# Kernel tuning notes

Measured on AMD Instinct MI355X. Metric: run time of the kernel, lower is better.

## Reference

```python
import jax, jax.numpy as jnp
import numpy as np

E = 2048        # embed_dim
HQ = 32         # num_query_heads
HKV = 8         # num_kv_heads
HD = E // HQ    # head_dim = 64
GROUP = HQ // HKV  # q_per_kv = 4
B, T = 2, 2048


def setup_inputs() -> dict:
    key = jax.random.key(0)
    ks = jax.random.split(key, 6)
    s = 0.02
    x  = jax.random.normal(ks[0], (B, T, E), dtype=jnp.float32)
    Wq = jax.random.normal(ks[1], (E, E), dtype=jnp.float32) * s
    Wk = jax.random.normal(ks[2], (E, HKV * HD), dtype=jnp.float32) * s
    Wv = jax.random.normal(ks[3], (E, HKV * HD), dtype=jnp.float32) * s
    Wo = jax.random.normal(ks[4], (E, E), dtype=jnp.float32) * s
    bo = jax.random.normal(ks[5], (E,), dtype=jnp.float32) * s
    return {"x": x, "Wq": Wq, "Wk": Wk, "Wv": Wv, "Wo": Wo, "bo": bo}


def reference(x, Wq, Wk, Wv, Wo, bo):
    Bc, Tc, _ = x.shape
    # projections
    q = (x @ Wq).reshape(Bc, Tc, HQ, HD).transpose(0, 2, 1, 3)      # [B,HQ,T,HD]
    k = (x @ Wk).reshape(Bc, Tc, HKV, HD).transpose(0, 2, 1, 3)     # [B,HKV,T,HD]
    v = (x @ Wv).reshape(Bc, Tc, HKV, HD).transpose(0, 2, 1, 3)     # [B,HKV,T,HD]
    # group queries by kv head instead of repeating k/v: [B,HKV,GROUP,T,HD]
    qg = q.reshape(Bc, HKV, GROUP, Tc, HD)
    scale = 1.0 / jnp.sqrt(jnp.asarray(HD, dtype=x.dtype))
    scores = jnp.einsum('bhgqd,bhkd->bhgqk', qg, k) * scale         # [B,HKV,GROUP,T,T]
    weights = jax.nn.softmax(scores, axis=-1)
    attn = jnp.einsum('bhgqk,bhkd->bhgqd', weights, v)              # [B,HKV,GROUP,T,HD]
    out = attn.reshape(Bc, HQ, Tc, HD).transpose(0, 2, 1, 3).reshape(Bc, Tc, E)
    return out @ Wo + bo
```

## Files before the change

kernel.cpp:

```cpp
#include <hip/hip_runtime.h>
#include <hip/hip_bf16.h>
#include <stdint.h>

#define E_ 2048
#define HQ_ 32
#define HKV_ 8
#define HD_ 64
#define B_ 2
#define T_ 2048
#define MROWS (B_*T_)
#define NKV (HKV_*HD_)
#define NQKV (E_ + 2*NKV)
#define SCALE_LOG2E 0.18033688011112042f

typedef __bf16 bf16_t;
typedef __bf16 bf16x8 __attribute__((ext_vector_type(8)));
typedef float f32x4 __attribute__((ext_vector_type(4)));
typedef float f32x16 __attribute__((ext_vector_type(16)));

typedef const __attribute__((address_space(1))) unsigned int glb_u32;
typedef __attribute__((address_space(3))) unsigned int lds_u32;

__device__ __forceinline__ unsigned short f2bf_bits(float f) {
  unsigned int u = __float_as_uint(f);
  u += 0x7FFFu + ((u >> 16) & 1u);
  return (unsigned short)(u >> 16);
}
__device__ __forceinline__ bf16_t f2bf(float f) {
  union { unsigned short s; bf16_t h; } u;
  u.s = f2bf_bits(f);
  return u.h;
}
__device__ __forceinline__ unsigned pack2bf(float lo, float hi) {
  union { struct { bf16_t l, h; } s; unsigned u; } c;
  c.s.l = (bf16_t)lo; c.s.h = (bf16_t)hi;
  return c.u;
}
__device__ __forceinline__ float fexp2(float x) {
#if __has_builtin(__builtin_amdgcn_exp2f)
  return __builtin_amdgcn_exp2f(x);
#else
  return exp2f(x);
#endif
}

__global__ void cast_x_kernel(const float* __restrict__ in, bf16_t* __restrict__ out, int n8) {
  int i = blockIdx.x * blockDim.x + threadIdx.x;
  int stride = gridDim.x * blockDim.x;
  for (; i < n8; i += stride) {
    const float4* p = reinterpret_cast<const float4*>(in) + (size_t)i * 2;
    float4 a = p[0], b = p[1];
    union { unsigned short s[8]; uint4 v; } u;
    u.s[0] = f2bf_bits(a.x); u.s[1] = f2bf_bits(a.y);
    u.s[2] = f2bf_bits(a.z); u.s[3] = f2bf_bits(a.w);
    u.s[4] = f2bf_bits(b.x); u.s[5] = f2bf_bits(b.y);
    u.s[6] = f2bf_bits(b.z); u.s[7] = f2bf_bits(b.w);
    reinterpret_cast<uint4*>(out)[i] = u.v;
  }
}

__global__ void transpose_cast_w(const float* __restrict__ in, bf16_t* __restrict__ out,
                                 int R, int C) {
  __shared__ float tile[32][33];
  int c0 = blockIdx.x * 32, r0 = blockIdx.y * 32;
  int tx = threadIdx.x, ty = threadIdx.y;
#pragma unroll
  for (int j = 0; j < 4; ++j) {
    int r = ty + j * 8;
    tile[r][tx] = in[(size_t)(r0 + r) * C + c0 + tx];
  }
  __syncthreads();
#pragma unroll
  for (int j = 0; j < 4; ++j) {
    int c = ty + j * 8;
    out[(size_t)(c0 + c) * R + r0 + tx] = f2bf(tile[tx][c]);
  }
}

__global__ void transpose_v_kernel(const bf16_t* __restrict__ qkv, bf16_t* __restrict__ vt) {
  __shared__ bf16_t tile[32][33];
  int b = blockIdx.z;
  int hd0 = blockIdx.x * 32, t0 = blockIdx.y * 32;
  int tx = threadIdx.x, ty = threadIdx.y;
#pragma unroll
  for (int j = 0; j < 4; ++j) {
    int tt = ty + j * 8;
    tile[tt][tx] = qkv[(size_t)(b * T_ + t0 + tt) * NQKV + (E_ + NKV) + hd0 + tx];
  }
  __syncthreads();
#pragma unroll
  for (int j = 0; j < 4; ++j) {
    int hh = ty + j * 8;
    vt[(size_t)(b * NKV + hd0 + hh) * T_ + t0 + tx] = tile[tx][hh];
  }
}

template <int OUTMODE>
__global__ void gemm_bt_kernel(const bf16_t* __restrict__ A, const bf16_t* __restrict__ BT,
                               void* __restrict__ Cv, const float* __restrict__ bias,
                               int M, int N, int K) {
  __shared__ bf16_t As[128 * 32];
  __shared__ bf16_t Bs[128 * 32];
  int tid = threadIdx.x;
  int w = tid >> 6, lane = tid & 63;
  int l15 = lane & 15, l4 = lane >> 4;
  int m0 = blockIdx.x * 128, n0 = blockIdx.y * 128;
  int wm = (w >> 1) * 64, wn = (w & 1) * 64;

  f32x4 zero = {0.f, 0.f, 0.f, 0.f};
  f32x4 acc[4][4];
#pragma unroll
  for (int mt = 0; mt < 4; ++mt)
#pragma unroll
    for (int nt = 0; nt < 4; ++nt) acc[mt][nt] = zero;

  int nK = K >> 5;
  for (int kt = 0; kt < nK; ++kt) {
    int k0 = kt << 5;
#pragma unroll
    for (int j = 0; j < 2; ++j) {
      int c = w * 2 + j;
      int L = c * 512 + lane * 8;
      int row = L >> 5, col = L & 31;
      __builtin_amdgcn_global_load_lds((glb_u32*)(A + (size_t)(m0 + row) * K + k0 + col),
                                       (lds_u32*)(As + c * 512), 16, 0, 0);
      __builtin_amdgcn_global_load_lds((glb_u32*)(BT + (size_t)(n0 + row) * K + k0 + col),
                                       (lds_u32*)(Bs + c * 512), 16, 0, 0);
    }
    __syncthreads();

    bf16x8 afr[4], bfr[4];
#pragma unroll
    for (int t = 0; t < 4; ++t) {
      afr[t] = *reinterpret_cast<const bf16x8*>(As + (wm + t * 16 + l15) * 32 + l4 * 8);
      bfr[t] = *reinterpret_cast<const bf16x8*>(Bs + (wn + t * 16 + l15) * 32 + l4 * 8);
    }
#pragma unroll
    for (int mt = 0; mt < 4; ++mt)
#pragma unroll
      for (int nt = 0; nt < 4; ++nt)
        acc[mt][nt] = __builtin_amdgcn_mfma_f32_16x16x32_bf16(afr[mt], bfr[nt], acc[mt][nt], 0, 0, 0);
    __syncthreads();
  }

  if (OUTMODE == 0) {
    bf16_t* C = reinterpret_cast<bf16_t*>(Cv);
#pragma unroll
    for (int mt = 0; mt < 4; ++mt)
#pragma unroll
      for (int nt = 0; nt < 4; ++nt) {
        int n = n0 + wn + nt * 16 + l15;
#pragma unroll
        for (int r = 0; r < 4; ++r) {
          int m = m0 + wm + mt * 16 + l4 * 4 + r;
          C[(size_t)m * N + n] = f2bf(acc[mt][nt][r]);
        }
      }
  } else {
    float* C = reinterpret_cast<float*>(Cv);
#pragma unroll
    for (int mt = 0; mt < 4; ++mt)
#pragma unroll
      for (int nt = 0; nt < 4; ++nt) {
        int n = n0 + wn + nt * 16 + l15;
        float bb = bias[n];
#pragma unroll
        for (int r = 0; r < 4; ++r) {
          int m = m0 + wm + mt * 16 + l4 * 4 + r;
          C[(size_t)m * N + n] = acc[mt][nt][r] + bb;
        }
      }
  }
}

__global__ void attn_kernel(const bf16_t* __restrict__ qkv, const bf16_t* __restrict__ vt,
                            bf16_t* __restrict__ attn) {
  __shared__ bf16_t Kbuf[2][64 * 64];
  __shared__ bf16_t Vbuf[2][64 * 64];
  __shared__ float bcast[8][32];

  int tid = threadIdx.x;
  int w = tid >> 6, lane = tid & 63;
  int l31 = lane & 31, hi = lane >> 5;
  int bh = blockIdx.y;
  int b = bh >> 5, hq = bh & 31, hkv = hq >> 2;
  int q0 = blockIdx.x * 256 + w * 32;

  bf16x8 qf[4];
  {
    const bf16_t* qp = qkv + (size_t)(b * T_ + q0 + l31) * NQKV + hq * HD_;
#pragma unroll
    for (int s = 0; s < 4; ++s) {
      bf16x8 q = *reinterpret_cast<const bf16x8*>(qp + s * 16 + hi * 8);
#pragma unroll
      for (int e = 0; e < 8; ++e) q[e] = (bf16_t)((float)q[e] * SCALE_LOG2E);
      qf[s] = q;
    }
  }

  f32x16 o0 = {0.f,0.f,0.f,0.f,0.f,0.f,0.f,0.f,0.f,0.f,0.f,0.f,0.f,0.f,0.f,0.f};
  f32x16 o1 = o0;
  float m_r = -1e30f, l_r = 0.f;

  int srow = w * 8 + (lane >> 3);
  int schunk = (lane & 7) ^ ((lane >> 3) & 7);
  const bf16_t* kg = qkv + (size_t)b * T_ * NQKV + E_ + hkv * HD_;
  const bf16_t* vg = vt + ((size_t)(b * HKV_ + hkv) * HD_ + srow) * T_;

#define STAGE_KV(bi, kv0) do {                                                          \
    __builtin_amdgcn_global_load_lds(                                                   \
        (glb_u32*)(kg + (size_t)((kv0) + srow) * NQKV + schunk * 8),                    \
        (lds_u32*)(&Kbuf[bi][w * 8 * 64]), 16, 0, 0);                                   \
    __builtin_amdgcn_global_load_lds(                                                   \
        (glb_u32*)(vg + (kv0) + schunk * 8),                                            \
        (lds_u32*)(&Vbuf[bi][w * 8 * 64]), 16, 0, 0);                                   \
  } while (0)

#define KREAD(bi, tsub, s) \
  (*reinterpret_cast<const bf16x8*>(&Kbuf[bi][((tsub) * 32 + l31) * 64 + \
      ((((s) * 2 + hi) ^ (l31 & 7)) * 8)]))
#define VREAD(bi, dh, s) \
  (*reinterpret_cast<const bf16x8*>(&Vbuf[bi][((dh) * 32 + l31) * 64 + \
      ((((s) * 2 + hi) ^ (l31 & 7)) * 8)]))

  STAGE_KV(0, 0);
  __syncthreads();

#pragma unroll 2
  for (int t = 0; t < T_ / 64; ++t) {
    int bi = t & 1;
    if (t < T_ / 64 - 1) STAGE_KV(bi ^ 1, (t + 1) * 64);

    f32x16 sa = {0.f,0.f,0.f,0.f,0.f,0.f,0.f,0.f,0.f,0.f,0.f,0.f,0.f,0.f,0.f,0.f};
    f32x16 sb = sa;
    __builtin_amdgcn_s_setprio(1);
#pragma unroll
    for (int s = 0; s < 4; ++s) {
      sa = __builtin_amdgcn_mfma_f32_32x32x16_bf16(KREAD(bi, 0, s), qf[s], sa, 0, 0, 0);
      sb = __builtin_amdgcn_mfma_f32_32x32x16_bf16(KREAD(bi, 1, s), qf[s], sb, 0, 0, 0);
    }
    __builtin_amdgcn_s_setprio(0);

    float pmax = sa[0];
#pragma unroll
    for (int r = 1; r < 16; ++r) pmax = fmaxf(pmax, sa[r]);
#pragma unroll
    for (int r = 0; r < 16; ++r) pmax = fmaxf(pmax, sb[r]);

    if (__any(pmax > m_r + 8.f)) {
      float pm2 = __shfl_xor(pmax, 32);
      float mnew = fmaxf(m_r, fmaxf(pmax, pm2));
      float corr = fexp2(m_r - mnew);
      m_r = mnew;
      l_r *= corr;
      bcast[w][l31] = corr;
      asm volatile("s_waitcnt lgkmcnt(0)" ::: "memory");
#pragma unroll
      for (int r = 0; r < 16; ++r) {
        float c = bcast[w][(r & 3) + 8 * (r >> 2) + 4 * hi];
        o0[r] *= c; o1[r] *= c;
      }
    }

    float pA[16], pB[16];
    float ps0 = 0.f, ps1 = 0.f;
#pragma unroll
    for (int r = 0; r < 16; ++r) {
      pA[r] = fexp2(sa[r] - m_r); ps0 += pA[r];
      pB[r] = fexp2(sb[r] - m_r); ps1 += pB[r];
    }
    l_r += ps0 + ps1;

    unsigned wd[2][4][2];
#pragma unroll
    for (int g = 0; g < 4; ++g)
#pragma unroll
      for (int j = 0; j < 2; ++j) {
        wd[0][g][j] = pack2bf(pA[4 * g + 2 * j], pA[4 * g + 2 * j + 1]);
        wd[1][g][j] = pack2bf(pB[4 * g + 2 * j], pB[4 * g + 2 * j + 1]);
      }

    __builtin_amdgcn_s_setprio(1);
#pragma unroll
    for (int s = 0; s < 4; ++s) {
      const int tt = s >> 1, gg = 2 * (s & 1);
      unsigned send0 = hi ? wd[tt][gg][0] : wd[tt][gg + 1][0];
      unsigned send1 = hi ? wd[tt][gg][1] : wd[tt][gg + 1][1];
      unsigned recv0 = __shfl_xor(send0, 32);
      unsigned recv1 = __shfl_xor(send1, 32);
      union { unsigned u[4]; bf16x8 v; } pf;
      pf.u[0] = hi ? recv0 : wd[tt][gg][0];
      pf.u[1] = hi ? recv1 : wd[tt][gg][1];
      pf.u[2] = hi ? wd[tt][gg + 1][0] : recv0;
      pf.u[3] = hi ? wd[tt][gg + 1][1] : recv1;
      o0 = __builtin_amdgcn_mfma_f32_32x32x16_bf16(pf.v, VREAD(bi, 0, s), o0, 0, 0, 0);
      o1 = __builtin_amdgcn_mfma_f32_32x32x16_bf16(pf.v, VREAD(bi, 1, s), o1, 0, 0, 0);
    }
    __builtin_amdgcn_s_setprio(0);

    __syncthreads();
  }
#undef STAGE_KV
#undef KREAD
#undef VREAD

  float lfull = l_r + __shfl_xor(l_r, 32);
  bcast[w][l31] = 1.0f / lfull;
  asm volatile("s_waitcnt lgkmcnt(0)" ::: "memory");
  const size_t obase = (size_t)(b * T_ + q0) * E_ + hq * HD_;
#pragma unroll
  for (int r = 0; r < 16; ++r) {
    int q = (r & 3) + 8 * (r >> 2) + 4 * hi;
    float rl = bcast[w][q];
    attn[obase + (size_t)q * E_ + l31]      = (bf16_t)(o0[r] * rl);
    attn[obase + (size_t)q * E_ + 32 + l31] = (bf16_t)(o1[r] * rl);
  }
}

extern "C" void kernel_launch(void* const* d_in, const int* in_sizes, int n_in,
                              void* d_out, int out_size, void* d_ws, size_t ws_size,
                              hipStream_t stream) {
  const float* x  = (const float*)d_in[0];
  const float* Wq = (const float*)d_in[1];
  const float* Wk = (const float*)d_in[2];
  const float* Wv = (const float*)d_in[3];
  const float* Wo = (const float*)d_in[4];
  const float* bo = (const float*)d_in[5];
  float* out = (float*)d_out;

  bf16_t* xb    = (bf16_t*)d_ws;
  bf16_t* WcatT = xb + (size_t)MROWS * E_;
  bf16_t* WoT   = WcatT + (size_t)NQKV * E_;
  bf16_t* QKV   = WoT + (size_t)E_ * E_;
  bf16_t* Vt    = QKV + (size_t)MROWS * NQKV;
  bf16_t* Attn  = Vt + (size_t)B_ * NKV * T_;

  dim3 tblk(32, 8);
  cast_x_kernel<<<2048, 256, 0, stream>>>(x, xb, MROWS * E_ / 8);
  transpose_cast_w<<<dim3(E_ / 32, E_ / 32), tblk, 0, stream>>>(Wq, WcatT, E_, E_);
  transpose_cast_w<<<dim3(NKV / 32, E_ / 32), tblk, 0, stream>>>(Wk, WcatT + (size_t)E_ * E_, E_, NKV);
  transpose_cast_w<<<dim3(NKV / 32, E_ / 32), tblk, 0, stream>>>(Wv, WcatT + (size_t)(E_ + NKV) * E_, E_, NKV);
  transpose_cast_w<<<dim3(E_ / 32, E_ / 32), tblk, 0, stream>>>(Wo, WoT, E_, E_);

  gemm_bt_kernel<0><<<dim3(MROWS / 128, NQKV / 128), 256, 0, stream>>>(
      xb, WcatT, (void*)QKV, nullptr, MROWS, NQKV, E_);

  transpose_v_kernel<<<dim3(NKV / 32, T_ / 32, B_), tblk, 0, stream>>>(QKV, Vt);

  attn_kernel<<<dim3(T_ / 256, B_ * HQ_), 512, 0, stream>>>(QKV, Vt, Attn);

  gemm_bt_kernel<1><<<dim3(MROWS / 128, E_ / 128), 256, 0, stream>>>(
      Attn, WoT, (void*)out, bo, MROWS, E_, E_);
}
```

Measured before the change: 381.8 us.

## Replace GEMM with double-buffered 256-row tiled 8-wave kernel using swizzled LDS

Result: no change. 375.2 us (-1.7%).

```diff
diff --git a/kernel.cpp b/kernel.cpp
--- a/kernel.cpp
+++ b/kernel.cpp
@@ -95,82 +95,149 @@
   }
 }
 
-template <int OUTMODE>
-__global__ void gemm_bt_kernel(const bf16_t* __restrict__ A, const bf16_t* __restrict__ BT,
-                               void* __restrict__ Cv, const float* __restrict__ bias,
-                               int M, int N, int K) {
-  __shared__ bf16_t As[128 * 32];
-  __shared__ bf16_t Bs[128 * 32];
-  int tid = threadIdx.x;
-  int w = tid >> 6, lane = tid & 63;
-  int l15 = lane & 15, l4 = lane >> 4;
-  int m0 = blockIdx.x * 128, n0 = blockIdx.y * 128;
-  int wm = (w >> 1) * 64, wn = (w & 1) * 64;
-
+#define VMW(n) asm volatile("s_waitcnt vmcnt(" #n ")" ::: "memory")
+#define BARSYNC do { asm volatile("" ::: "memory");            \
+                     __builtin_amdgcn_s_barrier();             \
+                     asm volatile("" ::: "memory"); } while (0)
+
+template <int BN, int OUTMODE>
+__global__ __launch_bounds__(512, 2)
+void gemm8_kernel(const bf16_t* __restrict__ A, const bf16_t* __restrict__ BT,
+                  void* __restrict__ Cv, const float* __restrict__ bias,
+                  int M, int N, int K) {
+  constexpr int BM = 256, BK = 64;
+  constexpr int WN = BN / 4;
+  constexpr int ACN = (BN == 256) ? 4 : 2;
+  __shared__ bf16_t As[2][BM * BK];
+  __shared__ bf16_t Bs[2][BN * BK];
+
+  const int tid = threadIdx.x;
+  const int wid = tid >> 6, lane = tid & 63;
+  const int l15 = lane & 15, l4 = lane >> 4;
+  const int wr = wid >> 2, wc = wid & 3;
+  const int m0 = blockIdx.x * BM, n0 = blockIdx.y * BN;
+  const int srow = lane >> 3;
+  const int schunk = (lane & 7) ^ srow;
+
+  f32x4 acc[8][ACN];
   f32x4 zero = {0.f, 0.f, 0.f, 0.f};
-  f32x4 acc[4][4];
-#pragma unroll
-  for (int mt = 0; mt < 4; ++mt)
-#pragma unroll
-    for (int nt = 0; nt < 4; ++nt) acc[mt][nt] = zero;
-
-  int nK = K >> 5;
+#pragma unroll
+  for (int i = 0; i < 8; ++i)
+#pragma unroll
+    for (int j = 0; j < ACN; ++j) acc[i][j] = zero;
+
+#define STAGE_A(nb, h, ktt) do {                                                        \
+    int k0s = (ktt) * BK;                                                               \
+    _Pragma("unroll") for (int j = 0; j < 2; ++j) {                                     \
+      int row0 = (h) * 64 + j * 128 + wid * 8;                                          \
+      __builtin_amdgcn_global_load_lds(                                                 \
+          (glb_u32*)(A + (size_t)(m0 + row0 + srow) * K + k0s + schunk * 8),            \
+          (lds_u32*)(&As[nb][row0 * 64]), 16, 0, 0);                                    \
+    } } while (0)
+
+#define STAGE_B2(nb, h, ktt) do {                                                       \
+    int k0s = (ktt) * BK;                                                               \
+    _Pragma("unroll") for (int j = 0; j < 2; ++j) {                                     \
+      int i0 = j * 64 + wid * 8;                                                        \
+      int row0 = (i0 & 31) + ((i0 >> 5) << 6) + (h) * 32;                               \
+      __builtin_amdgcn_global_load_lds(                                                 \
+          (glb_u32*)(BT + (size_t)(n0 + row0 + srow) * K + k0s + schunk * 8),           \
+          (lds_u32*)(&Bs[nb][row0 * 64]), 16, 0, 0);                                    \
+    } } while (0)
+
+#define STAGE_B1(nb, ktt) do {                                                          \
+    int k0s = (ktt) * BK;                                                               \
+    _Pragma("unroll") for (int j = 0; j < 2; ++j) {                                     \
+      int row0 = j * 64 + wid * 8;                                                      \
+      __builtin_amdgcn_global_load_lds(                                                 \
+          (glb_u32*)(BT + (size_t)(n0 + row0 + srow) * K + k0s + schunk * 8),           \
+          (lds_u32*)(&Bs[nb][row0 * 64]), 16, 0, 0);                                    \
+    } } while (0)
+
+  bf16x8 afr[4][2], bfr[2][2];
+#define LDA(mh) { _Pragma("unroll") for (int mf = 0; mf < 4; ++mf)                      \
+    _Pragma("unroll") for (int ks = 0; ks < 2; ++ks) {                                  \
+      int row = wr * 128 + (mh) * 64 + mf * 16 + l15;                                   \
+      afr[mf][ks] = *(const bf16x8*)&As[cur][row * 64 + ((ks * 4 + l4) ^ (l15 & 7)) * 8]; } }
+
+#define LDB(nh) { _Pragma("unroll") for (int nf = 0; nf < 2; ++nf)                      \
+    _Pragma("unroll") for (int ks = 0; ks < 2; ++ks) {                                  \
+      int row = wc * WN + (nh) * 32 + nf * 16 + l15;                                    \
+      bfr[nf][ks] = *(const bf16x8*)&Bs[cur][row * 64 + ((ks * 4 + l4) ^ (l15 & 7)) * 8]; } }
+
+#define MMA(mh, nh) {                                                                   \
+    __builtin_amdgcn_s_setprio(1);                                                      \
+    _Pragma("unroll") for (int ks = 0; ks < 2; ++ks)                                    \
+      _Pragma("unroll") for (int mf = 0; mf < 4; ++mf)                                  \
+        _Pragma("unroll") for (int nf = 0; nf < 2; ++nf)                                \
+          acc[(mh) * 4 + mf][(nh) * 2 + nf] = __builtin_amdgcn_mfma_f32_16x16x32_bf16(  \
+              afr[mf][ks], bfr[nf][ks], acc[(mh) * 4 + mf][(nh) * 2 + nf], 0, 0, 0);    \
+    __builtin_amdgcn_s_setprio(0); }
+
+  const int nK = K >> 6;
+
+  if (BN == 256) {
+    STAGE_A(0, 0, 0); STAGE_B2(0, 0, 0); STAGE_B2(0, 1, 0); STAGE_A(0, 1, 0);
+    VMW(4);
+  } else {
+    STAGE_A(0, 0, 0); STAGE_B1(0, 0);    STAGE_A(0, 1, 0);
+    VMW(2);
+  }
+  BARSYNC;
+
   for (int kt = 0; kt < nK; ++kt) {
-    int k0 = kt << 5;
-#pragma unroll
-    for (int j = 0; j < 2; ++j) {
-      int c = w * 2 + j;
-      int L = c * 512 + lane * 8;
-      int row = L >> 5, col = L & 31;
-      __builtin_amdgcn_global_load_lds((glb_u32*)(A + (size_t)(m0 + row) * K + k0 + col),
-                                       (lds_u32*)(As + c * 512), 16, 0, 0);
-      __builtin_amdgcn_global_load_lds((glb_u32*)(BT + (size_t)(n0 + row) * K + k0 + col),
-                                       (lds_u32*)(Bs + c * 512), 16, 0, 0);
-    }
-    __syncthreads();
-
-    bf16x8 afr[4], bfr[4];
-#pragma unroll
-    for (int t = 0; t < 4; ++t) {
-      afr[t] = *reinterpret_cast<const bf16x8*>(As + (wm + t * 16 + l15) * 32 + l4 * 8);
-      bfr[t] = *reinterpret_cast<const bf16x8*>(Bs + (wn + t * 16 + l15) * 32 + l4 * 8);
-    }
-#pragma unroll
-    for (int mt = 0; mt < 4; ++mt)
-#pragma unroll
-      for (int nt = 0; nt < 4; ++nt)
-        acc[mt][nt] = __builtin_amdgcn_mfma_f32_16x16x32_bf16(afr[mt], bfr[nt], acc[mt][nt], 0, 0, 0);
-    __syncthreads();
-  }
-
-  if (OUTMODE == 0) {
-    bf16_t* C = reinterpret_cast<bf16_t*>(Cv);
-#pragma unroll
-    for (int mt = 0; mt < 4; ++mt)
-#pragma unroll
-      for (int nt = 0; nt < 4; ++nt) {
-        int n = n0 + wn + nt * 16 + l15;
-#pragma unroll
-        for (int r = 0; r < 4; ++r) {
-          int m = m0 + wm + mt * 16 + l4 * 4 + r;
-          C[(size_t)m * N + n] = f2bf(acc[mt][nt][r]);
-        }
+    const int cur = kt & 1, nb = cur ^ 1;
+    const int ktn = (kt + 1 < nK) ? kt + 1 : 0;
+
+    if (BN == 256) {
+      LDA(0); LDB(0);
+      STAGE_A(nb, 0, ktn);
+      BARSYNC; MMA(0, 0); VMW(4); BARSYNC;
+      LDB(1);
+      STAGE_B2(nb, 0, ktn);
+      BARSYNC; MMA(0, 1); VMW(4); BARSYNC;
+      LDA(1);
+      STAGE_B2(nb, 1, ktn);
+      BARSYNC; MMA(1, 1); BARSYNC;
+      LDB(0);
+      STAGE_A(nb, 1, ktn);
+      BARSYNC; MMA(1, 0); VMW(4); BARSYNC;
+    } else {
+      LDA(0); LDB(0);
+      STAGE_A(nb, 0, ktn); STAGE_B1(nb, ktn);
+      BARSYNC; MMA(0, 0); VMW(4); BARSYNC;
+      LDA(1);
+      STAGE_A(nb, 1, ktn);
+      BARSYNC; MMA(1, 0); VMW(2); BARSYNC;
+    }
+  }
+  VMW(0);
+
+#pragma unroll
+  for (int mq = 0; mq < 8; ++mq)
+#pragma unroll
+    for (int nq = 0; nq < ACN; ++nq) {
+      int mrow = m0 + wr * 128 + (mq >> 2) * 64 + (mq & 3) * 16 + l4 * 4;
+      int ncol = n0 + wc * WN + (nq >> 1) * 32 + (nq & 1) * 16 + l15;
+      if (OUTMODE == 0) {
+        bf16_t* C = reinterpret_cast<bf16_t*>(Cv);
+#pragma unroll
+        for (int r = 0; r < 4; ++r)
+          C[(size_t)(mrow + r) * N + ncol] = f2bf(acc[mq][nq][r]);
+      } else {
+        float* C = reinterpret_cast<float*>(Cv);
+        float bb = bias[ncol];
+#pragma unroll
+        for (int r = 0; r < 4; ++r)
+          C[(size_t)(mrow + r) * N + ncol] = acc[mq][nq][r] + bb;
       }
-  } else {
-    float* C = reinterpret_cast<float*>(Cv);
-#pragma unroll
-    for (int mt = 0; mt < 4; ++mt)
-#pragma unroll
-      for (int nt = 0; nt < 4; ++nt) {
-        int n = n0 + wn + nt * 16 + l15;
-        float bb = bias[n];
-#pragma unroll
-        for (int r = 0; r < 4; ++r) {
-          int m = m0 + wm + mt * 16 + l4 * 4 + r;
-          C[(size_t)m * N + n] = acc[mt][nt][r] + bb;
-        }
-      }
-  }
+    }
+#undef STAGE_A
+#undef STAGE_B2
+#undef STAGE_B1
+#undef LDA
+#undef LDB
+#undef MMA
 }
 
 __global__ void attn_kernel(const bf16_t* __restrict__ qkv, const bf16_t* __restrict__ vt,
@@ -342,13 +409,13 @@
   transpose_cast_w<<<dim3(NKV / 32, E_ / 32), tblk, 0, stream>>>(Wv, WcatT + (size_t)(E_ + NKV) * E_, E_, NKV);
   transpose_cast_w<<<dim3(E_ / 32, E_ / 32), tblk, 0, stream>>>(Wo, WoT, E_, E_);
 
-  gemm_bt_kernel<0><<<dim3(MROWS / 128, NQKV / 128), 256, 0, stream>>>(
+  gemm8_kernel<256, 0><<<dim3(MROWS / 256, NQKV / 256), 512, 0, stream>>>(
       xb, WcatT, (void*)QKV, nullptr, MROWS, NQKV, E_);
 
   transpose_v_kernel<<<dim3(NKV / 32, T_ / 32, B_), tblk, 0, stream>>>(QKV, Vt);
 
   attn_kernel<<<dim3(T_ / 256, B_ * HQ_), 512, 0, stream>>>(QKV, Vt, Attn);
 
-  gemm_bt_kernel<1><<<dim3(MROWS / 128, E_ / 128), 256, 0, stream>>>(
+  gemm8_kernel<128, 1><<<dim3(MROWS / 256, E_ / 128), 512, 0, stream>>>(
       Attn, WoT, (void*)out, bo, MROWS, E_, E_);
 }
```
